# Kernel tuning notes

Hardware: AMD Instinct MI355X
Metric: run time of the kernel (lower is better)

## Reference

```python
import jax, jax.numpy as jnp
import numpy as np

PS = 8            # patch_size
GRID = 8          # img_size // patch_size
N_PATCHES = 64
PATCH_DIM = 192   # 3 * 8 * 8
CENTRAL = np.array([r * 8 + c for r in range(2, 6) for c in range(2, 6)], dtype=np.int32)  # 16 patches
AGENT = np.array([r * 8 + c for r in range(3, 6) for c in range(3, 6)], dtype=np.int32)    # 9 patches
EPS = 1e-8


def setup_inputs() -> dict:
    key = jax.random.key(0)
    k1, k2, k3, k4, k5 = jax.random.split(key, 5)
    B, K, E, V = 1024, 4096, 2048, 2048
    pixels = jax.random.uniform(k1, (B, 3, 64, 64), dtype=jnp.float32)
    codebook = jax.random.normal(k2, (K, PATCH_DIM), dtype=jnp.float32)
    codebook = codebook / jnp.clip(jnp.linalg.norm(codebook, axis=1, keepdims=True), EPS)
    embeddings = jax.random.normal(k3, (K, E), dtype=jnp.float32)
    codebook_vsa = jax.random.randint(k4, (K, V), 0, 2).astype(jnp.float32)
    position_roles = jax.random.randint(k5, (N_PATCHES, V), 0, 2).astype(jnp.float32)
    return {"pixels": pixels, "codebook": codebook, "embeddings": embeddings,
            "codebook_vsa": codebook_vsa, "position_roles": position_roles}


def _patchify(pixels):
    # (B,3,64,64) -> (B,64,192), matching torch unfold/permute order (gh, gw, C, ph, pw)
    B = pixels.shape[0]
    x = pixels.reshape(B, 3, GRID, PS, GRID, PS)          # (B,C,gh,ph,gw,pw)
    x = jnp.transpose(x, (0, 2, 4, 1, 3, 5))              # (B,gh,gw,C,ph,pw)
    return x.reshape(B, N_PATCHES, PATCH_DIM)


def reference(pixels, codebook, embeddings, codebook_vsa, position_roles):
    patches = _patchify(pixels)                                            # (B,64,192)
    patches_norm = patches / jnp.clip(
        jnp.linalg.norm(patches, axis=2, keepdims=True), EPS)
    sim = jnp.einsum('bpd,kd->bpk', patches_norm, codebook)                # (B,64,4096)
    indices = jnp.argmax(sim, axis=2)                                      # (B,64) int
    embeds = embeddings[indices]                                           # (B,64,2048)
    z_real = embeds.mean(axis=1)                                           # (B,2048)
    z_local = embeds[:, AGENT, :].mean(axis=1)                             # (B,2048)
    # VSA bind + bundle over the 16 central patches
    idx_c = indices[:, CENTRAL]                                            # (B,16)
    cb_vecs = codebook_vsa[idx_c]                                          # (B,16,V)
    pos = position_roles[CENTRAL]                                          # (16,V)
    bound = jnp.mod(cb_vecs + pos[None, :, :], 2.0)                        # XOR on {0,1}
    summed = bound.sum(axis=1)                                             # (B,V)
    z_vsa = (summed > (len(CENTRAL) / 2)).astype(jnp.float32)
    return z_real, z_vsa, indices, z_local
```

## Files before the change

kernel.cpp:

```cpp
#include <hip/hip_runtime.h>
#include <hip/hip_bf16.h>
#include <math.h>

#define NIMG 1024
#define NPATCH 64
#define PDIM 192
#define KCODES 4096
#define EDIM 2048
#define VDIM 2048
#define MROWS (NIMG * NPATCH)
#define KP 192
#define NKS 6
#define NCT 16

typedef _Float16 f16x8 __attribute__((ext_vector_type(8)));
typedef __attribute__((ext_vector_type(4))) float f32x4;

__device__ __forceinline__ void gload_lds16(const void* g, void* l) {
    __builtin_amdgcn_global_load_lds(
        (const __attribute__((address_space(1))) unsigned int*)g,
        (__attribute__((address_space(3))) unsigned int*)l,
        16, 0, 0);
}

__device__ __forceinline__ void merge_top2(float& v1, int& i1, float& v2, int& i2,
                                           float ov1, int oi1, float ov2, int oi2) {
    bool aw = (v1 > ov1) || (v1 == ov1 && i1 < oi1);
    float w1v = aw ? v1 : ov1;  int w1i = aw ? i1 : oi1;
    float c2v = aw ? v2 : ov2;  int c2i = aw ? i2 : oi2;
    float l1v = aw ? ov1 : v1;  int l1i = aw ? oi1 : i1;
    bool bw = (c2v > l1v) || (c2v == l1v && c2i < l1i);
    v1 = w1v; i1 = w1i;
    v2 = bw ? c2v : l1v; i2 = bw ? c2i : l1i;
}

__device__ __forceinline__ void kfold(int& t1, int& t2, int key) {
    int m = (key < t1) ? key : t1;
    t2 = (t2 > m) ? t2 : m;
    t1 = (t1 > key) ? t1 : key;
}

__global__ __launch_bounds__(256) void prep_patches_kernel(
    const float* __restrict__ pixels, unsigned short* __restrict__ Ah)
{
    __shared__ float inv[64];
    const int b = blockIdx.x, t = threadIdx.x;
    const float* pix = pixels + (size_t)b * 3 * 4096;
    if (t < 64) {
        int gr = t >> 3, gc = t & 7;
        const float* pb = pix + gr * 8 * 64 + gc * 8;
        float s = 0.f;
        #pragma unroll
        for (int ch = 0; ch < 3; ++ch)
            #pragma unroll
            for (int r = 0; r < 8; ++r)
                #pragma unroll
                for (int c = 0; c < 8; ++c) {
                    float x = pb[ch * 4096 + r * 64 + c];
                    s += x * x;
                }
        inv[t] = 1.f / fmaxf(sqrtf(s), 1e-8f);
    }
    __syncthreads();
    for (int i = t; i < 64 * 192; i += 256) {
        int p = i / 192, d = i - p * 192;
        int ch = d >> 6, r = (d >> 3) & 7, c = d & 7;
        int gr = p >> 3, gc = p & 7;
        float x = pix[ch * 4096 + (gr * 8 + r) * 64 + gc * 8 + c] * inv[p];
        _Float16 h = (_Float16)x;
        Ah[((size_t)b * 64 + p) * KP + d] = *(unsigned short*)&h;
    }
}

__global__ __launch_bounds__(256) void prep_codebook_kernel(
    const float* __restrict__ cb, unsigned short* __restrict__ Bh)
{
    int i = blockIdx.x * 256 + threadIdx.x;
    if (i >= KCODES * PDIM) return;
    _Float16 h = (_Float16)cb[i];
    Bh[i] = *(unsigned short*)&h;
}

__global__ __launch_bounds__(512) void gemm_top2_kernel(
    const unsigned short* __restrict__ A, const unsigned short* __restrict__ B,
    float* __restrict__ o1v, int* __restrict__ o1i,
    float* __restrict__ o2v, int* __restrict__ o2i)
{
    __shared__ unsigned short Asl[6][8192];
    __shared__ unsigned short Bsl[3][8192];

    const int t = threadIdx.x;
    const int w = t >> 6;
    const int l = t & 63;
    const int lo4 = l & 15, hi4 = l >> 4;
    const int wr = w >> 1, wc = w & 1;
    const int m0 = blockIdx.x * 256;

    const int srow = t >> 2;
    const int kc   = (t & 3) ^ ((srow >> 1) & 3);
    const unsigned short* a0b = A + (size_t)(m0 + srow) * KP + kc * 8;
    const unsigned short* b0b = B + (size_t)srow * KP + kc * 8;

    int aoff[4], boff[8];
    #pragma unroll
    for (int rt = 0; rt < 4; ++rt) {
        int row = wr * 64 + rt * 16 + lo4;
        aoff[rt] = row * 32 + (hi4 ^ ((row >> 1) & 3)) * 8;
    }
    #pragma unroll
    for (int cf = 0; cf < 8; ++cf) {
        int col = wc * 128 + cf * 16 + lo4;
        boff[cf] = col * 32 + (hi4 ^ ((col >> 1) & 3)) * 8;
    }

    int t1k[16], t2k[16];
    #pragma unroll
    for (int e = 0; e < 16; ++e) { t1k[e] = (int)0x80000000; t2k[e] = (int)0x80000000; }

    auto stageA = [&](int j) {
        char* Ad = (char*)Asl[j] + w * 1024;
        const unsigned short* ga = a0b + j * 32;
        gload_lds16(ga, Ad);
        gload_lds16(ga + 128 * KP, Ad + 8192);
    };
    auto stageB = [&](int sct, int sj, int sbuf) {
        char* Bd = (char*)Bsl[sbuf] + w * 1024;
        const unsigned short* gb = b0b + sct * (256 * KP) + sj * 32;
        gload_lds16(gb, Bd);
        gload_lds16(gb + 128 * KP, Bd + 8192);
    };

    #pragma unroll
    for (int j = 0; j < 6; ++j) stageA(j);
    stageB(0, 0, 0);
    stageB(0, 1, 1);
    asm volatile("s_waitcnt vmcnt(2)\n\ts_barrier" ::: "memory");

    f32x4 acc[4][8];
    int bb = 0, sb = 2;
    int stct = 0, stj = 2;

    for (int ct = 0; ct < NCT; ++ct) {
      for (int j = 0; j < NKS; ++j) {
        const unsigned short* Ab = Asl[j];
        const unsigned short* Bb = Bsl[bb];

        f16x8 af[4], bg[4];
        #pragma unroll
        for (int rt = 0; rt < 4; ++rt) af[rt] = *(const f16x8*)&Ab[aoff[rt]];
        #pragma unroll
        for (int cf = 0; cf < 4; ++cf) bg[cf] = *(const f16x8*)&Bb[boff[cf]];
        if (stct < NCT) stageB(stct, stj, sb);

        if (j == 0) {
            #pragma unroll
            for (int i = 0; i < 4; ++i)
                #pragma unroll
                for (int jj = 0; jj < 8; ++jj) acc[i][jj] = (f32x4){0.f, 0.f, 0.f, 0.f};
        }

        asm volatile("s_waitcnt lgkmcnt(0)" ::: "memory");
        __builtin_amdgcn_sched_barrier(0);
        __builtin_amdgcn_s_setprio(1);
        #pragma unroll
        for (int rt = 0; rt < 4; ++rt)
            #pragma unroll
            for (int cf = 0; cf < 4; ++cf)
                acc[rt][cf] = __builtin_amdgcn_mfma_f32_16x16x32_f16(af[rt], bg[cf], acc[rt][cf], 0, 0, 0);
        __builtin_amdgcn_s_setprio(0);

        f16x8 bh[4];
        #pragma unroll
        for (int cf = 0; cf < 4; ++cf) bh[cf] = *(const f16x8*)&Bb[boff[cf + 4]];

        asm volatile("s_waitcnt lgkmcnt(0)" ::: "memory");
        __builtin_amdgcn_sched_barrier(0);
        __builtin_amdgcn_s_setprio(1);
        #pragma unroll
        for (int rt = 0; rt < 4; ++rt)
            #pragma unroll
            for (int cf = 0; cf < 4; ++cf)
                acc[rt][cf + 4] = __builtin_amdgcn_mfma_f32_16x16x32_f16(af[rt], bh[cf], acc[rt][cf + 4], 0, 0, 0);
        __builtin_amdgcn_s_setprio(0);
        __builtin_amdgcn_sched_barrier(0);

        if (ct < NCT - 1 || j < NKS - 2) {
            asm volatile("s_waitcnt vmcnt(2)\n\ts_barrier" ::: "memory");
        } else if (j == NKS - 2) {
            asm volatile("s_waitcnt vmcnt(0)\n\ts_barrier" ::: "memory");
        }

        if (j == NKS - 1) {
            #pragma unroll
            for (int cf = 0; cf < 8; ++cf) {
                const int inv7 = 0x7F ^ ((ct << 3) | cf);
                #pragma unroll
                for (int rt = 0; rt < 4; ++rt)
                    #pragma unroll
                    for (int r = 0; r < 4; ++r) {
                        int key = (__float_as_int(acc[rt][cf][r]) & ~0x7F) | inv7;
                        kfold(t1k[rt * 4 + r], t2k[rt * 4 + r], key);
                    }
            }
        }

        if (stct < NCT && ++stj == NKS) { stj = 0; ++stct; }
        if (++bb == 3) bb = 0;
        if (++sb == 3) sb = 0;
      }
    }

    float p1v[16], p2v[16];
    int   p1i[16], p2i[16];
    #pragma unroll
    for (int e = 0; e < 16; ++e) {
        p1v[e] = __int_as_float(t1k[e] & ~0x7F);
        int lo7 = 0x7F ^ (t1k[e] & 0x7F);
        p1i[e] = ((lo7 >> 3) << 8) + wc * 128 + ((lo7 & 7) << 4) + lo4;
        p2v[e] = __int_as_float(t2k[e] & ~0x7F);
        int lo7b = 0x7F ^ (t2k[e] & 0x7F);
        p2i[e] = ((lo7b >> 3) << 8) + wc * 128 + ((lo7b & 7) << 4) + lo4;
    }

    #pragma unroll
    for (int e = 0; e < 16; ++e) {
        #pragma unroll
        for (int m = 1; m < 16; m <<= 1) {
            float ov1 = __shfl_xor(p1v[e], m);
            int   oi1 = __shfl_xor(p1i[e], m);
            float ov2 = __shfl_xor(p2v[e], m);
            int   oi2 = __shfl_xor(p2i[e], m);
            merge_top2(p1v[e], p1i[e], p2v[e], p2i[e], ov1, oi1, ov2, oi2);
        }
    }

    __syncthreads();
    float* r1v = (float*)Asl;
    float* r2v = r1v + 512;
    int*   r1i = (int*)(r2v + 512);
    int*   r2i = r1i + 512;
    if (lo4 == 0) {
        #pragma unroll
        for (int rt = 0; rt < 4; ++rt)
            #pragma unroll
            for (int r = 0; r < 4; ++r) {
                const int e = rt * 4 + r;
                int row = wr * 64 + rt * 16 + hi4 * 4 + r;
                r1v[row * 2 + wc] = p1v[e]; r1i[row * 2 + wc] = p1i[e];
                r2v[row * 2 + wc] = p2v[e]; r2i[row * 2 + wc] = p2i[e];
            }
    }
    __syncthreads();
    if (t < 256) {
        float v1 = r1v[t * 2], v2 = r2v[t * 2];
        int   i1 = r1i[t * 2], i2 = r2i[t * 2];
        merge_top2(v1, i1, v2, i2, r1v[t * 2 + 1], r1i[t * 2 + 1],
                                   r2v[t * 2 + 1], r2i[t * 2 + 1]);
        int grow = m0 + t;
        o1v[grow] = v1; o1i[grow] = i1;
        o2v[grow] = v2; o2i[grow] = i2;
    }
}

__global__ __launch_bounds__(256) void refine_kernel(
    const float* __restrict__ pixels, const float* __restrict__ codebook,
    const float* __restrict__ o1v, const int* __restrict__ o1i,
    const float* __restrict__ o2v, const int* __restrict__ o2i,
    int* __restrict__ idx_out, float* __restrict__ idxf_out)
{
    int row = blockIdx.x * 256 + threadIdx.x;
    if (row >= MROWS) return;
    float v1 = o1v[row], v2 = o2v[row];
    int   i1 = o1i[row], i2 = o2i[row];
    int idx = i1;
    if (v1 - v2 <= 4e-4f) {
        int b = row >> 6, p = row & 63;
        int gr = p >> 3, gc = p & 7;
        const float* pb = pixels + (size_t)b * 3 * 4096 + gr * 8 * 64 + gc * 8;
        const float* c1 = codebook + (size_t)i1 * PDIM;
        const float* c2 = codebook + (size_t)i2 * PDIM;
        double s1 = 0.0, s2 = 0.0;
        for (int d = 0; d < PDIM; ++d) {
            int ch = d >> 6, r = (d >> 3) & 7, c = d & 7;
            double x = (double)pb[ch * 4096 + r * 64 + c];
            s1 += x * (double)c1[d];
            s2 += x * (double)c2[d];
        }
        if (s2 > s1 || (s2 == s1 && i2 < i1)) idx = i2;
    }
    idx_out[row] = idx;
    idxf_out[row] = (float)idx;
}

__global__ __launch_bounds__(256) void zv_kernel(
    const float* __restrict__ emb, const float* __restrict__ vsa,
    const float* __restrict__ roles, const int* __restrict__ idx,
    float* __restrict__ z_real, float* __restrict__ z_local,
    float* __restrict__ z_vsa)
{
    __shared__ int sidx[64];
    int b = blockIdx.x, t = threadIdx.x;
    if (t < 64) sidx[t] = idx[b * 64 + t];
    __syncthreads();
    float s[8], sl[8];
    #pragma unroll
    for (int j = 0; j < 8; ++j) { s[j] = 0.f; sl[j] = 0.f; }
    for (int p = 0; p < 64; ++p) {
        int gr = p >> 3, gc = p & 7;
        bool ag = (gr >= 3 && gr < 6 && gc >= 3 && gc < 6);
        const float* er = emb + (size_t)sidx[p] * EDIM + t * 8;
        float v[8];
        *(float4*)&v[0] = *(const float4*)er;
        *(float4*)&v[4] = *(const float4*)(er + 4);
        #pragma unroll
        for (int j = 0; j < 8; ++j) s[j] += v[j];
        if (ag) {
            #pragma unroll
            for (int j = 0; j < 8; ++j) sl[j] += v[j];
        }
    }
    float* zr = z_real + (size_t)b * EDIM + t * 8;
    float* zl = z_local + (size_t)b * EDIM + t * 8;
    #pragma unroll
    for (int j = 0; j < 8; ++j) {
        zr[j] = s[j] * (1.f / 64.f);
        zl[j] = sl[j] * (1.f / 9.f);
    }

    float cnt[8];
    #pragma unroll
    for (int j = 0; j < 8; ++j) cnt[j] = 0.f;
    for (int cp = 0; cp < 16; ++cp) {
        int p = (2 + (cp >> 2)) * 8 + 2 + (cp & 3);
        const float* vr = vsa + (size_t)sidx[p] * VDIM + t * 8;
        const float* pr = roles + (size_t)p * VDIM + t * 8;
        float a[8], r[8];
        *(float4*)&a[0] = *(const float4*)vr;
        *(float4*)&a[4] = *(const float4*)(vr + 4);
        *(float4*)&r[0] = *(const float4*)pr;
        *(float4*)&r[4] = *(const float4*)(pr + 4);
        #pragma unroll
        for (int j = 0; j < 8; ++j) cnt[j] += (a[j] != r[j]) ? 1.f : 0.f;
    }
    #pragma unroll
    for (int j = 0; j < 8; ++j)
        z_vsa[(size_t)b * VDIM + t * 8 + j] = cnt[j] > 8.f ? 1.f : 0.f;
}

extern "C" void kernel_launch(void* const* d_in, const int* in_sizes, int n_in,
                              void* d_out, int out_size, void* d_ws, size_t ws_size,
                              hipStream_t stream) {
    const float* pixels         = (const float*)d_in[0];
    const float* codebook       = (const float*)d_in[1];
    const float* embeddings     = (const float*)d_in[2];
    const float* codebook_vsa   = (const float*)d_in[3];
    const float* position_roles = (const float*)d_in[4];

    float* out     = (float*)d_out;
    float* z_real  = out;
    float* z_vsa   = out + 2097152;
    float* idxf    = out + 4194304;
    float* z_local = out + 4259840;

    char* ws = (char*)d_ws;
    unsigned short* Ah = (unsigned short*)(ws);
    unsigned short* Bh = (unsigned short*)(ws + 25165824);
    float* o1v = (float*)(ws + 26738688);
    int*   o1i = (int*)  (ws + 27000832);
    float* o2v = (float*)(ws + 27262976);
    int*   o2i = (int*)  (ws + 27525120);
    int*   idxws = (int*)(ws + 27787264);

    prep_patches_kernel<<<NIMG, 256, 0, stream>>>(pixels, Ah);
    prep_codebook_kernel<<<(KCODES * PDIM + 255) / 256, 256, 0, stream>>>(codebook, Bh);

    gemm_top2_kernel<<<MROWS / 256, 512, 0, stream>>>(Ah, Bh, o1v, o1i, o2v, o2i);

    refine_kernel<<<MROWS / 256, 256, 0, stream>>>(pixels, codebook,
        o1v, o1i, o2v, o2i, idxws, idxf);
    zv_kernel<<<NIMG, 256, 0, stream>>>(embeddings, codebook_vsa, position_roles,
        idxws, z_real, z_local, z_vsa);
}
```

Measured before the change: 208.9 us.

## Shrink GEMM-top2 block tile to 128 rows and raise occupancy

Each GEMM block now covers 128 rows instead of 256, with 4 column-waves of 64 columns each and half the accumulators per wave. LDS use drops: the A tile is halved and B goes from a triple to a double buffer. launch_bounds(512,4) asks for more resident blocks per CU to hide latency. In exchange, B tiles are reloaded by twice as many blocks, the pipeline has less prefetch depth, there is a full vmcnt(0) barrier every k-step, and the top-2 merge across waves gets wider.

```diff
diff --git a/kernel.cpp b/kernel.cpp
--- a/kernel.cpp
+++ b/kernel.cpp
@@ -81,35 +81,35 @@
     Bh[i] = *(unsigned short*)&h;
 }
 
-__global__ __launch_bounds__(512) void gemm_top2_kernel(
+__global__ __launch_bounds__(512, 4) void gemm_top2_kernel(
     const unsigned short* __restrict__ A, const unsigned short* __restrict__ B,
     float* __restrict__ o1v, int* __restrict__ o1i,
     float* __restrict__ o2v, int* __restrict__ o2i)
 {
-    __shared__ unsigned short Asl[6][8192];
-    __shared__ unsigned short Bsl[3][8192];
+    __shared__ unsigned short Asl[6][4096];
+    __shared__ unsigned short Bsl[2][8192];
 
     const int t = threadIdx.x;
     const int w = t >> 6;
     const int l = t & 63;
     const int lo4 = l & 15, hi4 = l >> 4;
-    const int wr = w >> 1, wc = w & 1;
-    const int m0 = blockIdx.x * 256;
+    const int wr = w >> 2, wc = w & 3;
+    const int m0 = blockIdx.x * 128;
 
     const int srow = t >> 2;
     const int kc   = (t & 3) ^ ((srow >> 1) & 3);
     const unsigned short* a0b = A + (size_t)(m0 + srow) * KP + kc * 8;
     const unsigned short* b0b = B + (size_t)srow * KP + kc * 8;
 
-    int aoff[4], boff[8];
+    int aoff[4], boff[4];
     #pragma unroll
     for (int rt = 0; rt < 4; ++rt) {
         int row = wr * 64 + rt * 16 + lo4;
         aoff[rt] = row * 32 + (hi4 ^ ((row >> 1) & 3)) * 8;
     }
     #pragma unroll
-    for (int cf = 0; cf < 8; ++cf) {
-        int col = wc * 128 + cf * 16 + lo4;
+    for (int cf = 0; cf < 4; ++cf) {
+        int col = wc * 64 + cf * 16 + lo4;
         boff[cf] = col * 32 + (hi4 ^ ((col >> 1) & 3)) * 8;
     }
 
@@ -118,10 +118,7 @@
     for (int e = 0; e < 16; ++e) { t1k[e] = (int)0x80000000; t2k[e] = (int)0x80000000; }
 
     auto stageA = [&](int j) {
-        char* Ad = (char*)Asl[j] + w * 1024;
-        const unsigned short* ga = a0b + j * 32;
-        gload_lds16(ga, Ad);
-        gload_lds16(ga + 128 * KP, Ad + 8192);
+        gload_lds16(a0b + j * 32, (char*)Asl[j] + w * 1024);
     };
     auto stageB = [&](int sct, int sj, int sbuf) {
         char* Bd = (char*)Bsl[sbuf] + w * 1024;
@@ -133,93 +130,68 @@
     #pragma unroll
     for (int j = 0; j < 6; ++j) stageA(j);
     stageB(0, 0, 0);
-    stageB(0, 1, 1);
-    asm volatile("s_waitcnt vmcnt(2)\n\ts_barrier" ::: "memory");
-
-    f32x4 acc[4][8];
-    int bb = 0, sb = 2;
-    int stct = 0, stj = 2;
+    asm volatile("s_waitcnt vmcnt(0)\n\ts_barrier" ::: "memory");
+
+    f32x4 acc[4][4];
 
     for (int ct = 0; ct < NCT; ++ct) {
-      for (int j = 0; j < NKS; ++j) {
-        const unsigned short* Ab = Asl[j];
-        const unsigned short* Bb = Bsl[bb];
-
-        f16x8 af[4], bg[4];
-        #pragma unroll
-        for (int rt = 0; rt < 4; ++rt) af[rt] = *(const f16x8*)&Ab[aoff[rt]];
-        #pragma unroll
-        for (int cf = 0; cf < 4; ++cf) bg[cf] = *(const f16x8*)&Bb[boff[cf]];
-        if (stct < NCT) stageB(stct, stj, sb);
-
-        if (j == 0) {
-            #pragma unroll
-            for (int i = 0; i < 4; ++i)
+        #pragma unroll
+        for (int j = 0; j < NKS; ++j) {
+            if (j < NKS - 1)          stageB(ct, j + 1, (j + 1) & 1);
+            else if (ct < NCT - 1)    stageB(ct + 1, 0, 0);
+
+            const unsigned short* Ab = Asl[j];
+            const unsigned short* Bb = Bsl[j & 1];
+            f16x8 af[4], bg[4];
+            #pragma unroll
+            for (int rt = 0; rt < 4; ++rt) af[rt] = *(const f16x8*)&Ab[aoff[rt]];
+            #pragma unroll
+            for (int cf = 0; cf < 4; ++cf) bg[cf] = *(const f16x8*)&Bb[boff[cf]];
+
+            if (j == 0) {
                 #pragma unroll
-                for (int jj = 0; jj < 8; ++jj) acc[i][jj] = (f32x4){0.f, 0.f, 0.f, 0.f};
-        }
-
-        asm volatile("s_waitcnt lgkmcnt(0)" ::: "memory");
-        __builtin_amdgcn_sched_barrier(0);
-        __builtin_amdgcn_s_setprio(1);
-        #pragma unroll
-        for (int rt = 0; rt < 4; ++rt)
-            #pragma unroll
-            for (int cf = 0; cf < 4; ++cf)
-                acc[rt][cf] = __builtin_amdgcn_mfma_f32_16x16x32_f16(af[rt], bg[cf], acc[rt][cf], 0, 0, 0);
-        __builtin_amdgcn_s_setprio(0);
-
-        f16x8 bh[4];
-        #pragma unroll
-        for (int cf = 0; cf < 4; ++cf) bh[cf] = *(const f16x8*)&Bb[boff[cf + 4]];
-
-        asm volatile("s_waitcnt lgkmcnt(0)" ::: "memory");
-        __builtin_amdgcn_sched_barrier(0);
-        __builtin_amdgcn_s_setprio(1);
-        #pragma unroll
-        for (int rt = 0; rt < 4; ++rt)
-            #pragma unroll
-            for (int cf = 0; cf < 4; ++cf)
-                acc[rt][cf + 4] = __builtin_amdgcn_mfma_f32_16x16x32_f16(af[rt], bh[cf], acc[rt][cf + 4], 0, 0, 0);
-        __builtin_amdgcn_s_setprio(0);
-        __builtin_amdgcn_sched_barrier(0);
-
-        if (ct < NCT - 1 || j < NKS - 2) {
-            asm volatile("s_waitcnt vmcnt(2)\n\ts_barrier" ::: "memory");
-        } else if (j == NKS - 2) {
-            asm volatile("s_waitcnt vmcnt(0)\n\ts_barrier" ::: "memory");
-        }
-
-        if (j == NKS - 1) {
-            #pragma unroll
-            for (int cf = 0; cf < 8; ++cf) {
-                const int inv7 = 0x7F ^ ((ct << 3) | cf);
+                for (int i = 0; i < 4; ++i)
+                    #pragma unroll
+                    for (int jj = 0; jj < 4; ++jj) acc[i][jj] = (f32x4){0.f, 0.f, 0.f, 0.f};
+            }
+
+            __builtin_amdgcn_s_setprio(1);
+            #pragma unroll
+            for (int rt = 0; rt < 4; ++rt)
                 #pragma unroll
-                for (int rt = 0; rt < 4; ++rt)
+                for (int cf = 0; cf < 4; ++cf)
+                    acc[rt][cf] = __builtin_amdgcn_mfma_f32_16x16x32_f16(af[rt], bg[cf], acc[rt][cf], 0, 0, 0);
+            __builtin_amdgcn_s_setprio(0);
+
+            if (ct < NCT - 1 || j < NKS - 1)
+                asm volatile("s_waitcnt vmcnt(0) lgkmcnt(0)\n\ts_barrier" ::: "memory");
+
+            if (j == NKS - 1) {
+                #pragma unroll
+                for (int cf = 0; cf < 4; ++cf) {
+                    const int inv6 = 0x3F ^ ((ct << 2) | cf);
                     #pragma unroll
-                    for (int r = 0; r < 4; ++r) {
-                        int key = (__float_as_int(acc[rt][cf][r]) & ~0x7F) | inv7;
-                        kfold(t1k[rt * 4 + r], t2k[rt * 4 + r], key);
-                    }
+                    for (int rt = 0; rt < 4; ++rt)
+                        #pragma unroll
+                        for (int r = 0; r < 4; ++r) {
+                            int key = (__float_as_int(acc[rt][cf][r]) & ~0x3F) | inv6;
+                            kfold(t1k[rt * 4 + r], t2k[rt * 4 + r], key);
+                        }
+                }
             }
         }
-
-        if (stct < NCT && ++stj == NKS) { stj = 0; ++stct; }
-        if (++bb == 3) bb = 0;
-        if (++sb == 3) sb = 0;
-      }
     }
 
     float p1v[16], p2v[16];
     int   p1i[16], p2i[16];
     #pragma unroll
     for (int e = 0; e < 16; ++e) {
-        p1v[e] = __int_as_float(t1k[e] & ~0x7F);
-        int lo7 = 0x7F ^ (t1k[e] & 0x7F);
-        p1i[e] = ((lo7 >> 3) << 8) + wc * 128 + ((lo7 & 7) << 4) + lo4;
-        p2v[e] = __int_as_float(t2k[e] & ~0x7F);
-        int lo7b = 0x7F ^ (t2k[e] & 0x7F);
-        p2i[e] = ((lo7b >> 3) << 8) + wc * 128 + ((lo7b & 7) << 4) + lo4;
+        p1v[e] = __int_as_float(t1k[e] & ~0x3F);
+        int e6 = 0x3F ^ (t1k[e] & 0x3F);
+        p1i[e] = (e6 >> 2) * 256 + wc * 64 + (e6 & 3) * 16 + lo4;
+        p2v[e] = __int_as_float(t2k[e] & ~0x3F);
+        int e6b = 0x3F ^ (t2k[e] & 0x3F);
+        p2i[e] = (e6b >> 2) * 256 + wc * 64 + (e6b & 3) * 16 + lo4;
     }
 
     #pragma unroll
@@ -246,16 +218,18 @@
             for (int r = 0; r < 4; ++r) {
                 const int e = rt * 4 + r;
                 int row = wr * 64 + rt * 16 + hi4 * 4 + r;
-                r1v[row * 2 + wc] = p1v[e]; r1i[row * 2 + wc] = p1i[e];
-                r2v[row * 2 + wc] = p2v[e]; r2i[row * 2 + wc] = p2i[e];
+                r1v[row * 4 + wc] = p1v[e]; r1i[row * 4 + wc] = p1i[e];
+                r2v[row * 4 + wc] = p2v[e]; r2i[row * 4 + wc] = p2i[e];
             }
     }
     __syncthreads();
-    if (t < 256) {
-        float v1 = r1v[t * 2], v2 = r2v[t * 2];
-        int   i1 = r1i[t * 2], i2 = r2i[t * 2];
-        merge_top2(v1, i1, v2, i2, r1v[t * 2 + 1], r1i[t * 2 + 1],
-                                   r2v[t * 2 + 1], r2i[t * 2 + 1]);
+    if (t < 128) {
+        float v1 = r1v[t * 4], v2 = r2v[t * 4];
+        int   i1 = r1i[t * 4], i2 = r2i[t * 4];
+        #pragma unroll
+        for (int q = 1; q < 4; ++q)
+            merge_top2(v1, i1, v2, i2, r1v[t * 4 + q], r1i[t * 4 + q],
+                                       r2v[t * 4 + q], r2i[t * 4 + q]);
         int grow = m0 + t;
         o1v[grow] = v1; o1i[grow] = i1;
         o2v[grow] = v2; o2i[grow] = i2;
@@ -374,7 +348,7 @@
     prep_patches_kernel<<<NIMG, 256, 0, stream>>>(pixels, Ah);
     prep_codebook_kernel<<<(KCODES * PDIM + 255) / 256, 256, 0, stream>>>(codebook, Bh);
 
-    gemm_top2_kernel<<<MROWS / 256, 512, 0, stream>>>(Ah, Bh, o1v, o1i, o2v, o2i);
+    gemm_top2_kernel<<<MROWS / 128, 512, 0, stream>>>(Ah, Bh, o1v, o1i, o2v, o2i);
 
     refine_kernel<<<MROWS / 256, 256, 0, stream>>>(pixels, codebook,
         o1v, o1i, o2v, o2i, idxws, idxf);
```

Result: slower. 271.1 us (+29.8%).
